# Kernel tuning notes

Hardware: AMD Instinct MI355X
Metric: run time of the kernel (lower is better)

The kernel has to match this reference:

```python
import jax, jax.numpy as jnp
import numpy as np

B, C, H, W = 8, 80, 128, 128
K = 100
MAX_OBJS = 128
N_GT = 256  # 32 GT boxes per image
HM_W, WH_W, OFF_W = 1.0, 0.1, 1.0
BETA = 0.1  # iou_map weight ('Ct IoU Loss x 0.1')


def setup_inputs() -> dict:
    key = jax.random.key(0)
    ks = jax.random.split(key, 12)
    hm = jax.random.normal(ks[0], (B, C, H, W), jnp.float32)
    wh = jax.random.normal(ks[1], (B, 2, H, W), jnp.float32) * 2.0 + 8.0
    reg = jax.random.normal(ks[2], (B, 2, H, W), jnp.float32) * 0.1
    hm_target = jax.random.uniform(ks[3], (B, C, H, W), jnp.float32) * 0.99
    wh_target = jax.random.uniform(ks[4], (B, MAX_OBJS, 2), jnp.float32) * 20.0 + 2.0
    reg_target = jax.random.uniform(ks[5], (B, MAX_OBJS, 2), jnp.float32)
    reg_mask = jax.random.randint(ks[6], (B, MAX_OBJS), 0, 2).astype(jnp.int32)
    ind = jax.random.randint(ks[7], (B, MAX_OBJS), 0, H * W).astype(jnp.int32)
    cx = jax.random.uniform(ks[8], (N_GT,)) * (W - 1)
    cy = jax.random.uniform(ks[9], (N_GT,)) * (H - 1)
    bw = jax.random.uniform(ks[10], (N_GT,)) * 30.0 + 2.0
    bh = jax.random.uniform(ks[11], (N_GT,)) * 30.0 + 2.0
    target_box = jnp.stack([cx - bw / 2, cy - bh / 2, cx + bw / 2, cy + bh / 2], -1).astype(jnp.float32)
    target_bidx = jnp.repeat(jnp.arange(B), N_GT // B).astype(jnp.int32)
    return {"hm": hm, "wh": wh, "reg": reg, "hm_target": hm_target,
            "wh_target": wh_target, "reg_target": reg_target,
            "reg_mask": reg_mask, "ind": ind,
            "target_box": target_box, "target_bidx": target_bidx}


def _gather_feat(feat, ind):
    # feat [B, ch, H, W], ind [B, M] spatial indices -> [B, M, ch]
    b, ch = feat.shape[0], feat.shape[1]
    f = feat.reshape(b, ch, -1).transpose(0, 2, 1)  # [B, HW, ch]
    return jnp.take_along_axis(f, ind[:, :, None], axis=1)


def _pairwise_iou(boxes1, boxes2):
    # boxes1 [K,4], boxes2 [N,4], xyxy -> [K,N]
    a1 = jnp.maximum(boxes1[:, 2] - boxes1[:, 0], 0.0) * jnp.maximum(boxes1[:, 3] - boxes1[:, 1], 0.0)
    a2 = jnp.maximum(boxes2[:, 2] - boxes2[:, 0], 0.0) * jnp.maximum(boxes2[:, 3] - boxes2[:, 1], 0.0)
    lt = jnp.maximum(boxes1[:, None, :2], boxes2[None, :, :2])
    rb = jnp.minimum(boxes1[:, None, 2:], boxes2[None, :, 2:])
    whi = jnp.clip(rb - lt, 0.0)
    inter = whi[..., 0] * whi[..., 1]
    union = a1[:, None] + a2[None, :] - inter
    return inter / jnp.maximum(union, 1e-7)


def _decode(hm_s, wh, reg):
    # _nms: 3x3 max-pool peak keeping
    hmax = jax.lax.reduce_window(hm_s, -jnp.inf, jax.lax.max,
                                 (1, 1, 3, 3), (1, 1, 1, 1),
                                 [(0, 0), (0, 0), (1, 1), (1, 1)])
    hm_k = jnp.where(hmax == hm_s, hm_s, 0.0)
    # global top-K over C*H*W (equivalent to per-class topK then topK-of-topK)
    scores, inds = jax.lax.top_k(hm_k.reshape(B, -1), K)
    clses = inds // (H * W)
    sinds = inds % (H * W)
    ys_i = sinds // W
    xs_i = sinds % W
    r = _gather_feat(reg, sinds)  # [B,K,2] sub-pixel offsets
    xs = xs_i.astype(jnp.float32) + r[..., 0]
    ys = ys_i.astype(jnp.float32) + r[..., 1]
    w = _gather_feat(wh, sinds)   # [B,K,2]
    boxes = jnp.stack([xs - w[..., 0] / 2, ys - w[..., 1] / 2,
                       xs + w[..., 0] / 2, ys + w[..., 1] / 2], -1)
    return boxes, scores, clses, ys_i, xs_i


def _focal_loss(pred, gt):
    # CenterNet focal loss; pred already sigmoid+clamped
    pos = gt == 1.0
    neg_w = (1.0 - gt) ** 4
    pos_loss = jnp.sum(jnp.where(pos, jnp.log(pred) * (1.0 - pred) ** 2, 0.0))
    neg_loss = jnp.sum(jnp.where(pos, 0.0, jnp.log(1.0 - pred) * pred ** 2 * neg_w))
    num_pos = jnp.sum(pos.astype(jnp.float32))
    return jnp.where(num_pos > 0, -(pos_loss + neg_loss) / jnp.maximum(num_pos, 1.0), -neg_loss)


def _reg_l1(out, mask, ind, tgt):
    pred = _gather_feat(out, ind)                       # [B, M, 2]
    m = jnp.broadcast_to(mask.astype(jnp.float32)[:, :, None], pred.shape)
    return jnp.sum(jnp.abs(pred * m - tgt * m)) / (jnp.sum(m) + 1e-4)


def reference(hm, wh, reg, hm_target, wh_target, reg_target, reg_mask, ind, target_box, target_bidx):
    hm_s = jnp.clip(jax.nn.sigmoid(hm), 1e-4, 1.0 - 1e-4)  # _sigmoid
    boxes, scores, clses, ys_i, xs_i = _decode(hm_s, wh, reg)
    # per-image pairwise IoU vs GT boxes of the same image, max over GT
    iou_all = jax.vmap(lambda bx: _pairwise_iou(bx, target_box))(boxes)  # [B,K,N]
    bmask = target_bidx[None, None, :] == jnp.arange(B)[:, None, None]
    iou = jnp.max(jnp.where(bmask, iou_all, 0.0), axis=-1)              # [B,K]
    # scatter IoU into dense heatmap-shaped iou_map at (b, cls, y, x)
    b_idx = jnp.broadcast_to(jnp.arange(B)[:, None], (B, K))
    iou_map = jnp.zeros_like(hm_s).at[b_idx, clses, ys_i, xs_i].set(iou)
    hm_t = jnp.clip(hm_target + BETA * iou_map, 0.0, 1.0)
    hm_loss = _focal_loss(hm_s, hm_t)
    wh_loss = _reg_l1(wh, reg_mask, ind, wh_target)
    off_loss = _reg_l1(reg, reg_mask, ind, reg_target)
    loss = HM_W * hm_loss + WH_W * wh_loss + OFF_W * off_loss
    return loss, hm_loss, wh_loss, off_loss
```

## Files before the change

kernel.cpp:

```cpp
#include <hip/hip_runtime.h>
#include <math.h>

#define B_ 8
#define C_ 80
#define H_ 128
#define W_ 128
#define K_ 100
#define MAXOBJS_ 128
#define NGT_ 256
#define HW_ (H_*W_)
#define CHW_ (C_*H_*W_)
#define TOT_ (B_*CHW_)
#define NBINS_ 4096
#define BCAP_ 4096
#define DCAP_ 128
#define CAPLDS_ 1024
#define DLOC_ 128
#define BLOC_ 768
#define NEGINF_ (-INFINITY)

#define OFF_MISC    64
#define OFF_LISTCNT 96
#define OFF_BDONE   128
#define OFF_SELDONE 160
#define OFF_THRB    192
#define OFF_CNTA    224
#define OFF_CNTB    256
#define OFF_HIST    512
#define ZERO_BYTES  131584
#define OFF_DEFV    131584
#define OFF_DEFI    135680
#define OFF_BORV    139776
#define OFF_BORI    270848
#define OFF_LIST    401920
#define CAP_REQ     196608ull
#define CAP_MAX     262144ull

__device__ __forceinline__ unsigned skey(float x){
    unsigned u = __float_as_uint(x);
    return (u & 0x80000000u) ? ~u : (u | 0x80000000u);
}

__device__ __forceinline__ void find_thr(const unsigned* __restrict__ lh,
                                         unsigned* __restrict__ part,
                                         unsigned target,
                                         unsigned* out_thr, unsigned* out_cum){
    int t = threadIdx.x;
    unsigned s = 0;
    #pragma unroll
    for(int k=0;k<16;++k) s += lh[t*16+k];
    part[t] = s;
    __syncthreads();
    for(int off=1; off<256; off<<=1){
        unsigned v = (t+off<256) ? part[t+off] : 0u;
        __syncthreads();
        part[t] += v;
        __syncthreads();
    }
    unsigned nxt = (t<255) ? part[t+1] : 0u;
    if(part[t] >= target && nxt < target){
        unsigned cum = nxt;
        int thr = t*16;
        for(int bin=t*16+15; bin>=t*16; --bin){
            unsigned c = lh[bin];
            if(cum + c >= target){ thr = bin; break; }
            cum += c;
        }
        *out_thr = (unsigned)thr;
        *out_cum = cum;
    }
    __syncthreads();
}

__device__ __forceinline__ void hmax4v(const float4& f, float le, float re, float h[4]){
    h[0]=fmaxf(fmaxf(le,  f.x), f.y);
    h[1]=fmaxf(fmaxf(f.x, f.y), f.z);
    h[2]=fmaxf(fmaxf(f.y, f.z), f.w);
    h[3]=fmaxf(fmaxf(f.z, f.w), re);
}

__global__ __launch_bounds__(256) void k_main(const float* __restrict__ hm,
        const float* __restrict__ hmt, unsigned* __restrict__ hist,
        double* __restrict__ accum, unsigned* __restrict__ listcnt,
        int2* __restrict__ list, int capB){
    __shared__ unsigned lh[NBINS_];
    __shared__ int2 lbuf[CAPLDS_];
    __shared__ float wsum[4];
    __shared__ unsigned lcnt, lbase;
    int t = threadIdx.x;
    int plane = blockIdx.x >> 1;
    int half  = blockIdx.x & 1;
    int b = plane / C_;
    int cls = plane - b*C_;
    const float* P = hm  + (size_t)plane*HW_;
    const float* T = hmt + (size_t)plane*HW_;
    int idx0 = cls*HW_;

    for(int i=t;i<NBINS_;i+=256) lh[i]=0u;
    if(t==0) lcnt=0u;
    __syncthreads();

    int xq = t & 31;
    int y0 = half*64 + (t>>5)*8;

    float4 rows[10];
    #pragma unroll
    for(int r=0;r<10;++r){
        int y = y0 - 1 + r;
        if(y >= 0 && y < H_) rows[r] = *(const float4*)(P + y*W_ + xq*4);
        else { rows[r].x=NEGINF_; rows[r].y=NEGINF_; rows[r].z=NEGINF_; rows[r].w=NEGINF_; }
    }
    float4 tgt[8];
    #pragma unroll
    for(int r=0;r<8;++r) tgt[r] = *(const float4*)(T + (y0+r)*W_ + xq*4);

    float le[10], re[10];
    #pragma unroll
    for(int r=0;r<10;++r){
        float l  = __shfl_up(rows[r].w, 1, 32);
        float rr = __shfl_down(rows[r].x, 1, 32);
        le[r] = (xq==0)  ? NEGINF_ : l;
        re[r] = (xq==31) ? NEGINF_ : rr;
    }

    float acc = 0.f;
    #pragma unroll
    for(int ri=0; ri<8; ++ri){
        int r = ri + 1;
        int y = y0 + ri;
        float vv[4] = {rows[r].x, rows[r].y, rows[r].z, rows[r].w};
        float hp[4]; hmax4v(rows[r-1], le[r-1], re[r-1], hp);
        float hn[4]; hmax4v(rows[r+1], le[r+1], re[r+1], hn);
        float lrv[4];
        lrv[0]=fmaxf(le[r], vv[1]);
        lrv[1]=fmaxf(vv[0], vv[2]);
        lrv[2]=fmaxf(vv[1], vv[3]);
        lrv[3]=fmaxf(vv[2], re[r]);
        float tgv[4] = {tgt[ri].x, tgt[ri].y, tgt[ri].z, tgt[ri].w};
        #pragma unroll
        for(int j=0;j<4;++j){
            float v = vv[j];
            bool pk = (v>=lrv[j]) && (v>=hp[j]) && (v>=hn[j]);
            if(pk){
                atomicAdd(&lh[skey(v)>>20], 1u);
                if(capB){
                    unsigned p = atomicAdd(&lcnt, 1u);
                    int2 e; e.x = __float_as_int(v); e.y = idx0 + y*W_ + xq*4 + j;
                    if(p < CAPLDS_) lbuf[p] = e;
                    else {
                        unsigned g = atomicAdd(&listcnt[b], 1u);
                        if(g < (unsigned)capB) list[(size_t)b*capB + g] = e;
                    }
                }
            }
            float pr = 1.f/(1.f + __expf(-v));
            pr = fminf(fmaxf(pr, 1e-4f), 1.f - 1e-4f);
            float q = 1.f - tgv[j]; float q2 = q*q;
            acc += __logf(1.f - pr) * pr * pr * q2 * q2;
        }
    }
    __syncthreads();

    unsigned n = lcnt; if(n > CAPLDS_) n = CAPLDS_;
    if(capB && t==0) lbase = atomicAdd(&listcnt[b], n);
    for(int i=t;i<NBINS_;i+=256){ unsigned c=lh[i]; if(c) atomicAdd(&hist[b*NBINS_+i], c); }
    #pragma unroll
    for(int off=32; off>0; off>>=1) acc += __shfl_xor(acc, off, 64);
    if((t & 63) == 0) wsum[t>>6] = acc;
    __syncthreads();
    if(capB){
        for(unsigned i=t;i<n;i+=256){
            unsigned g = lbase + i;
            if(g < (unsigned)capB) list[(size_t)b*capB + g] = lbuf[i];
        }
    }
    if(t==0) atomicAdd(&accum[0], (double)(wsum[0]+wsum[1]+wsum[2]+wsum[3]));
}

__global__ void k_thresh(const unsigned* __restrict__ hist, unsigned* __restrict__ thrbin){
    __shared__ unsigned lh[NBINS_];
    __shared__ unsigned part[256];
    __shared__ unsigned thrs, cums;
    int b = blockIdx.x, t = threadIdx.x;
    for(int i=t;i<NBINS_;i+=256) lh[i]=hist[b*NBINS_+i];
    if(t==0){ thrs=0u; cums=0u; }
    __syncthreads();
    find_thr(lh, part, (unsigned)K_, &thrs, &cums);
    if(t==0) thrbin[b]=thrs;
}

__global__ __launch_bounds__(256) void k_scan(const int2* __restrict__ list,
        const unsigned* __restrict__ listcnt, int capB,
        const unsigned* __restrict__ thrbin,
        unsigned* __restrict__ cntA, unsigned* __restrict__ cntB,
        float* __restrict__ defv, int* __restrict__ defi,
        float* __restrict__ borv, int* __restrict__ bori){
    __shared__ int2 dloc[DLOC_];
    __shared__ int2 bloc[BLOC_];
    __shared__ unsigned dc, bc, dbase, bbase;
    int b = blockIdx.x >> 6;
    int chunk = blockIdx.x & 63;
    int t = threadIdx.x;
    if(t==0){ dc=0u; bc=0u; }
    __syncthreads();
    unsigned thr = thrbin[b];
    unsigned n = listcnt[b]; if(n > (unsigned)capB) n = (unsigned)capB;
    for(unsigned i = chunk*256u + t; i < n; i += 64u*256u){
        int2 e = list[(size_t)b*capB + i];
        float v = __int_as_float(e.x);
        unsigned bin = skey(v) >> 20;
        if(bin > thr){
            unsigned p = atomicAdd(&dc, 1u);
            if(p < DLOC_) dloc[p] = e;
            else { unsigned g = atomicAdd(&cntA[b],1u); if(g<DCAP_){ defv[b*DCAP_+g]=v; defi[b*DCAP_+g]=e.y; } }
        } else if(bin == thr){
            unsigned p = atomicAdd(&bc, 1u);
            if(p < BLOC_) bloc[p] = e;
            else { unsigned g = atomicAdd(&cntB[b],1u); if(g<BCAP_){ borv[b*BCAP_+g]=v; bori[b*BCAP_+g]=e.y; } }
        }
    }
    __syncthreads();
    unsigned dn = dc < DLOC_ ? dc : DLOC_;
    unsigned bn = bc < BLOC_ ? bc : BLOC_;
    if(t==0){
        dbase = dn ? atomicAdd(&cntA[b], dn) : 0u;
        bbase = bn ? atomicAdd(&cntB[b], bn) : 0u;
    }
    __syncthreads();
    for(unsigned i=t;i<dn;i+=256){
        unsigned g = dbase + i;
        if(g < DCAP_){ defv[b*DCAP_+g]=__int_as_float(dloc[i].x); defi[b*DCAP_+g]=dloc[i].y; }
    }
    for(unsigned i=t;i<bn;i+=256){
        unsigned g = bbase + i;
        if(g < BCAP_){ borv[b*BCAP_+g]=__int_as_float(bloc[i].x); bori[b*BCAP_+g]=bloc[i].y; }
    }
}

__device__ __forceinline__ bool is_peak_scalar(const float* __restrict__ hm, int idx, float v){
    int w = idx & (W_-1);
    int h = (idx >> 7) & (H_-1);
    bool peak = true;
    #pragma unroll
    for(int dy=-1; dy<=1; ++dy){
        int hh = h + dy;
        if(hh < 0 || hh >= H_) continue;
        #pragma unroll
        for(int dx=-1; dx<=1; ++dx){
            if(dy==0 && dx==0) continue;
            int ww = w + dx;
            if(ww < 0 || ww >= W_) continue;
            peak = peak && (v >= __ldg(&hm[idx + dy*W_ + dx]));
        }
    }
    return peak;
}

__global__ __launch_bounds__(256) void k_collect(const float* __restrict__ hm,
        const unsigned* __restrict__ thrbin,
        unsigned* __restrict__ cntA, unsigned* __restrict__ cntB,
        float* __restrict__ defv, int* __restrict__ defi,
        float* __restrict__ borv, int* __restrict__ bori){
    int idx = blockIdx.x*256 + threadIdx.x;
    float v = hm[idx];
    if(!is_peak_scalar(hm, idx, v)) return;
    int b = idx / CHW_;
    unsigned bin = skey(v) >> 20;
    unsigned thr = thrbin[b];
    if(bin > thr){
        unsigned p = atomicAdd(&cntA[b], 1u);
        if(p < DCAP_){ defv[b*DCAP_+p] = v; defi[b*DCAP_+p] = idx - b*CHW_; }
    } else if(bin == thr){
        unsigned p = atomicAdd(&cntB[b], 1u);
        if(p < BCAP_){ borv[b*BCAP_+p] = v; bori[b*BCAP_+p] = idx - b*CHW_; }
    }
}

__global__ __launch_bounds__(256) void k_select(const float* __restrict__ hm,
        const float* __restrict__ hmt, const float* __restrict__ wh,
        const float* __restrict__ reg, const float* __restrict__ tbox,
        const int* __restrict__ tbid,
        const float* __restrict__ wht, const float* __restrict__ regt,
        const int* __restrict__ mask, const int* __restrict__ ind,
        const unsigned* __restrict__ cntA, const unsigned* __restrict__ cntB,
        const float* __restrict__ defv, const int* __restrict__ defi,
        const float* __restrict__ borv, const int* __restrict__ bori,
        double* __restrict__ accum, int* __restrict__ misc,
        unsigned* __restrict__ seldone, float* __restrict__ out){
    int b = blockIdx.x, t = threadIdx.x;
    __shared__ float gbox[NGT_][4];
    __shared__ float garea[NGT_];
    __shared__ float sv[BCAP_];
    __shared__ int   si[BCAP_];
    __shared__ unsigned h2[NBINS_];
    __shared__ unsigned t4[BCAP_];
    __shared__ unsigned part[256];
    __shared__ int  rvI[256];
    __shared__ int  sel[K_];
    __shared__ float sbx[K_][4];
    __shared__ float sa[K_];
    __shared__ int   ioui[K_];
    __shared__ float r0s[256], r1s[256], r2s[256];
    __shared__ unsigned gcnt, selc, t3c, t4c;
    __shared__ unsigned thr2s, cum2s, thr3s, need3s;
    __shared__ int wsel, amlast;

    int nA = (int)cntA[b]; if(nA>DCAP_) nA=DCAP_; if(nA>K_) nA=K_;
    int nB = (int)cntB[b]; if(nB>BCAP_) nB=BCAP_;
    int m = K_ - nA; if(m>nB) m=nB; if(m<0) m=0;

    if(t==0){ gcnt=0u; selc=(unsigned)nA; t3c=0u; t4c=0u;
              thr2s=0u; cum2s=0u; thr3s=0u; need3s=0u; }
    for(int i=t;i<NBINS_;i+=256) h2[i]=0u;
    __syncthreads();

    for(int i=t;i<NGT_;i+=256){
        if(tbid[i]==b){
            unsigned p = atomicAdd(&gcnt, 1u);
            float gx1=tbox[i*4+0], gy1=tbox[i*4+1], gx2=tbox[i*4+2], gy2=tbox[i*4+3];
            gbox[p][0]=gx1; gbox[p][1]=gy1; gbox[p][2]=gx2; gbox[p][3]=gy2;
            garea[p]=fmaxf(gx2-gx1,0.f)*fmaxf(gy2-gy1,0.f);
        }
    }
    for(int i=t;i<nB;i+=256){ sv[i]=borv[b*BCAP_+i]; si[i]=bori[b*BCAP_+i]; }
    for(int i=t;i<nA;i+=256) sel[i]=defi[b*DCAP_+i];
    __syncthreads();

    if(m>0){
        for(int i=t;i<nB;i+=256) atomicAdd(&h2[(skey(sv[i])>>8)&0xFFFu], 1u);
        __syncthreads();
        find_thr(h2, part, (unsigned)m, &thr2s, &cum2s);
        unsigned thr2 = thr2s, need2 = (unsigned)m - cum2s;
        for(int i=t;i<nB;i+=256){
            unsigned sb=(skey(sv[i])>>8)&0xFFFu;
            if(sb>thr2){ unsigned p=atomicAdd(&selc,1u); if(p<K_) sel[p]=si[i]; }
            else if(sb==thr2){ unsigned p=atomicAdd(&t3c,1u); if(p<BCAP_) t4[p]=(unsigned)i; }
        }
        __syncthreads();
        unsigned nt3=t3c; if(nt3>BCAP_) nt3=BCAP_;
        part[t]=0u;
        __syncthreads();
        for(unsigned i=t;i<nt3;i+=256) atomicAdd(&part[skey(sv[t4[i]])&0xFFu], 1u);
        __syncthreads();
        for(int off=1; off<256; off<<=1){
            unsigned v = (t+off<256)? part[t+off] : 0u;
            __syncthreads();
            part[t] += v;
            __syncthreads();
        }
        {
            unsigned nxt = (t<255)? part[t+1] : 0u;
            if(part[t] >= need2 && nxt < need2){ thr3s=(unsigned)t; need3s=need2-nxt; }
        }
        __syncthreads();
        unsigned thr3=thr3s, need3=need3s;
        for(unsigned i=t;i<nt3;i+=256){
            unsigned ci=t4[i];
            unsigned lb=skey(sv[ci])&0xFFu;
            if(lb>thr3){ unsigned p=atomicAdd(&selc,1u); if(p<K_) sel[p]=si[ci]; }
            else if(lb==thr3){ unsigned p=atomicAdd(&t4c,1u); if(p<NBINS_) h2[p]=(unsigned)si[ci]; }
        }
        __syncthreads();
        unsigned n4=t4c; if(n4>NBINS_) n4=NBINS_;
        if(need3 >= n4){
            for(unsigned i=t;i<n4;i+=256){ unsigned p=atomicAdd(&selc,1u); if(p<K_) sel[p]=(int)h2[i]; }
            __syncthreads();
        } else {
            for(unsigned it=0; it<need3; ++it){
                int bi=0x7FFFFFFF;
                for(unsigned i=t;i<n4;i+=256){ int w=(int)h2[i]; bi = (w<bi)?w:bi; }
                rvI[t]=bi;
                __syncthreads();
                for(int st=128;st>0;st>>=1){
                    if(t<st){ int w=rvI[t+st]; if(w<rvI[t]) rvI[t]=w; }
                    __syncthreads();
                }
                if(t==0){ wsel=rvI[0]; unsigned p=selc; selc=p+1u; if(p<K_) sel[p]=wsel; }
                __syncthreads();
                int w=wsel;
                for(unsigned i=t;i<n4;i+=256) if((int)h2[i]==w) h2[i]=0x7FFFFFFFu;
                __syncthreads();
            }
        }
    }
    __syncthreads();

    int nsel=(int)selc; if(nsel>K_) nsel=K_;
    for(int k=t;k<nsel;k+=256){
        int idx = sel[k];
        int cls = idx / HW_;
        int sp  = idx - cls*HW_;
        int yi = sp>>7, xi = sp&(W_-1);
        float rr0 = reg[(b*2+0)*HW_+sp], rr1 = reg[(b*2+1)*HW_+sp];
        float w0 = wh[(b*2+0)*HW_+sp],  w1 = wh[(b*2+1)*HW_+sp];
        float xs = (float)xi + rr0, ys = (float)yi + rr1;
        float x1=xs-w0*0.5f, y1=ys-w1*0.5f, x2=xs+w0*0.5f, y2=ys+w1*0.5f;
        sbx[k][0]=x1; sbx[k][1]=y1; sbx[k][2]=x2; sbx[k][3]=y2;
        sa[k] = fmaxf(x2-x1,0.f)*fmaxf(y2-y1,0.f);
        ioui[k] = 0;
    }
    __syncthreads();
    int ng = (int)gcnt; if(ng>NGT_) ng=NGT_;
    for(int pi=t; pi<nsel*ng; pi+=256){
        int k = pi / ng, g = pi - k*ng;
        float x1=sbx[k][0], y1=sbx[k][1], x2=sbx[k][2], y2=sbx[k][3];
        float ix1=fmaxf(x1,gbox[g][0]), iy1=fmaxf(y1,gbox[g][1]);
        float ix2=fminf(x2,gbox[g][2]), iy2=fminf(y2,gbox[g][3]);
        float iw=fmaxf(ix2-ix1,0.f), ih=fmaxf(iy2-iy1,0.f);
        float inter=iw*ih;
        float uni = sa[k] + garea[g] - inter;
        float iou = inter / fmaxf(uni, 1e-7f);
        atomicMax(&ioui[k], __float_as_int(iou));
    }
    __syncthreads();
    for(int k=t;k<nsel;k+=256){
        float best = __int_as_float(ioui[k]);
        int gidx = b*CHW_ + sel[k];
        float v = hm[gidx];
        float p = 1.f/(1.f + __expf(-v));
        p = fminf(fmaxf(p, 1e-4f), 1.f - 1e-4f);
        float gt0 = hmt[gidx];
        float q0 = 1.f - gt0; float q02 = q0*q0;
        float neg0 = __logf(1.f - p) * p * p * q02 * q02;
        float gt1 = fminf(gt0 + 0.1f*best, 1.f);
        if(gt1 == 1.f){
            atomicAdd(&misc[0], 1);
            float op = 1.f - p;
            atomicAdd(&accum[1], (double)(__logf(p)*op*op));
            atomicAdd(&accum[2], (double)(-neg0));
        } else {
            float q1 = 1.f - gt1; float q12 = q1*q1;
            float neg1 = __logf(1.f - p) * p * p * q12 * q12;
            atomicAdd(&accum[2], (double)(neg1 - neg0));
        }
    }

    __threadfence();
    __syncthreads();
    if(t==0){
        unsigned d = atomicAdd(seldone, 1u);
        amlast = (d == (unsigned)(B_-1));
    }
    __syncthreads();
    if(amlast){
        __threadfence();
        float whn=0.f, offn=0.f, ms=0.f;
        for(int i=t;i<B_*MAXOBJS_;i+=256){
            int bb = i >> 7;
            float mk = (float)mask[i];
            int id = ind[i];
            float p0 = wh[(bb*2+0)*HW_+id], p1 = wh[(bb*2+1)*HW_+id];
            whn += mk*(fabsf(p0 - wht[2*i]) + fabsf(p1 - wht[2*i+1]));
            float q0 = reg[(bb*2+0)*HW_+id], q1 = reg[(bb*2+1)*HW_+id];
            offn += mk*(fabsf(q0 - regt[2*i]) + fabsf(q1 - regt[2*i+1]));
            ms += 2.f*mk;
        }
        r0s[t]=whn; r1s[t]=offn; r2s[t]=ms;
        __syncthreads();
        for(int st=128; st>0; st>>=1){
            if(t<st){ r0s[t]+=r0s[t+st]; r1s[t]+=r1s[t+st]; r2s[t]+=r2s[t+st]; }
            __syncthreads();
        }
        if(t==0){
            double nb  = __hip_atomic_load(&accum[0], __ATOMIC_RELAXED, __HIP_MEMORY_SCOPE_AGENT);
            double pos = __hip_atomic_load(&accum[1], __ATOMIC_RELAXED, __HIP_MEMORY_SCOPE_AGENT);
            double nd  = __hip_atomic_load(&accum[2], __ATOMIC_RELAXED, __HIP_MEMORY_SCOPE_AGENT);
            int np = __hip_atomic_load(&misc[0], __ATOMIC_RELAXED, __HIP_MEMORY_SCOPE_AGENT);
            double neg = nb + nd;
            float hm_loss = (np > 0) ? (float)(-(pos + neg)/(double)np) : (float)(-neg);
            float msum = r2s[0];
            float wh_loss  = r0s[0] / (msum + 1e-4f);
            float off_loss = r1s[0] / (msum + 1e-4f);
            out[0] = hm_loss + 0.1f*wh_loss + off_loss;
            out[1] = hm_loss; out[2] = wh_loss; out[3] = off_loss;
        }
    }
}

extern "C" void kernel_launch(void* const* d_in, const int* in_sizes, int n_in,
                              void* d_out, int out_size, void* d_ws, size_t ws_size,
                              hipStream_t stream){
    const float* hm   = (const float*)d_in[0];
    const float* wh   = (const float*)d_in[1];
    const float* reg  = (const float*)d_in[2];
    const float* hmt  = (const float*)d_in[3];
    const float* wht  = (const float*)d_in[4];
    const float* regt = (const float*)d_in[5];
    const int*   mask = (const int*)d_in[6];
    const int*   ind  = (const int*)d_in[7];
    const float* tbox = (const float*)d_in[8];
    const int*   tbid = (const int*)d_in[9];

    char* ws = (char*)d_ws;
    double*   accum   = (double*)ws;
    int*      misc    = (int*)(ws + OFF_MISC);
    unsigned* listcnt = (unsigned*)(ws + OFF_LISTCNT);
    unsigned* seldone = (unsigned*)(ws + OFF_SELDONE);
    unsigned* thrbin  = (unsigned*)(ws + OFF_THRB);
    unsigned* cntA    = (unsigned*)(ws + OFF_CNTA);
    unsigned* cntB    = (unsigned*)(ws + OFF_CNTB);
    unsigned* hist    = (unsigned*)(ws + OFF_HIST);
    float*    defv    = (float*)(ws + OFF_DEFV);
    int*      defi    = (int*)(ws + OFF_DEFI);
    float*    borv    = (float*)(ws + OFF_BORV);
    int*      bori    = (int*)(ws + OFF_BORI);
    int2*     list    = (int2*)(ws + OFF_LIST);

    size_t capB = 0;
    if(ws_size >= (size_t)OFF_LIST + CAP_REQ*(size_t)B_*8ull){
        capB = (ws_size - (size_t)OFF_LIST) / ((size_t)B_*8ull);
        if(capB > CAP_MAX) capB = CAP_MAX;
    }

    hipMemsetAsync(ws, 0, ZERO_BYTES, stream);
    k_main<<<B_*C_*2, 256, 0, stream>>>(hm, hmt, hist, accum, listcnt, list, (int)capB);
    k_thresh<<<B_, 256, 0, stream>>>(hist, thrbin);
    if(capB){
        k_scan<<<B_*64, 256, 0, stream>>>(list, listcnt, (int)capB, thrbin,
                                          cntA, cntB, defv, defi, borv, bori);
    } else {
        k_collect<<<TOT_/256, 256, 0, stream>>>(hm, thrbin, cntA, cntB,
                                                defv, defi, borv, bori);
    }
    k_select<<<B_, 256, 0, stream>>>(hm, hmt, wh, reg, tbox, tbid,
                                     wht, regt, mask, ind, cntA, cntB,
                                     defv, defi, borv, bori, accum, misc,
                                     seldone, (float*)d_out);
    (void)in_sizes; (void)n_in; (void)out_size;
}
```

Baseline: 81.41 us.

## Split fused focal-loss and peak-detection kernel into separate kernels

The fused main kernel is split into two. k_focal is a grid-stride elementwise kernel that computes the negative focal-loss sum over hm and hm_target. k_peaks does 3x3 peak detection on quarter-plane tiles of 4 rows per thread, using a rolling row window and scalar halo loads in place of shuffles. The aim is to lower register pressure and raise occupancy and parallelism, at the cost of reading hm twice and adding one kernel launch.

```diff
diff --git a/kernel.cpp b/kernel.cpp
--- a/kernel.cpp
+++ b/kernel.cpp
@@ -14,14 +14,14 @@
 #define NBINS_ 4096
 #define BCAP_ 4096
 #define DCAP_ 128
-#define CAPLDS_ 1024
+#define QCAP_ 512
 #define DLOC_ 128
 #define BLOC_ 768
+#define FBLK_ 2048
 #define NEGINF_ (-INFINITY)
 
 #define OFF_MISC    64
 #define OFF_LISTCNT 96
-#define OFF_BDONE   128
 #define OFF_SELDONE 160
 #define OFF_THRB    192
 #define OFF_CNTA    224
@@ -72,28 +72,68 @@
     __syncthreads();
 }
 
-__device__ __forceinline__ void hmax4v(const float4& f, float le, float re, float h[4]){
-    h[0]=fmaxf(fmaxf(le,  f.x), f.y);
-    h[1]=fmaxf(fmaxf(f.x, f.y), f.z);
-    h[2]=fmaxf(fmaxf(f.y, f.z), f.w);
-    h[3]=fmaxf(fmaxf(f.z, f.w), re);
-}
-
-__global__ __launch_bounds__(256) void k_main(const float* __restrict__ hm,
-        const float* __restrict__ hmt, unsigned* __restrict__ hist,
-        double* __restrict__ accum, unsigned* __restrict__ listcnt,
+__global__ __launch_bounds__(256) void k_focal(const float* __restrict__ hm,
+        const float* __restrict__ hmt, double* __restrict__ accum){
+    __shared__ float wsum[4];
+    int t = threadIdx.x;
+    float acc = 0.f;
+    const float4* __restrict__ v4p = (const float4*)hm;
+    const float4* __restrict__ t4p = (const float4*)hmt;
+    for(int i = blockIdx.x*256 + t; i < TOT_/4; i += FBLK_*256){
+        float4 v4 = v4p[i];
+        float4 g4 = t4p[i];
+        float vv[4] = {v4.x, v4.y, v4.z, v4.w};
+        float gg[4] = {g4.x, g4.y, g4.z, g4.w};
+        #pragma unroll
+        for(int j=0;j<4;++j){
+            float v = vv[j];
+            float p = 1.f/(1.f + __expf(-v));
+            p = fminf(fmaxf(p, 1e-4f), 1.f - 1e-4f);
+            float q = 1.f - gg[j]; float q2 = q*q;
+            acc += __logf(1.f - p) * p * p * q2 * q2;
+        }
+    }
+    #pragma unroll
+    for(int off=32; off>0; off>>=1) acc += __shfl_xor(acc, off, 64);
+    if((t & 63) == 0) wsum[t>>6] = acc;
+    __syncthreads();
+    if(t==0) atomicAdd(&accum[0], (double)(wsum[0]+wsum[1]+wsum[2]+wsum[3]));
+}
+
+struct Row { float v[4]; float le, re; };
+
+__device__ __forceinline__ Row loadrow(const float* __restrict__ P, int y, int xq){
+    Row r;
+    if(y < 0 || y >= H_){
+        r.v[0]=r.v[1]=r.v[2]=r.v[3]=r.le=r.re=NEGINF_;
+        return r;
+    }
+    const float4 f = *(const float4*)(P + y*W_ + xq*4);
+    r.v[0]=f.x; r.v[1]=f.y; r.v[2]=f.z; r.v[3]=f.w;
+    r.le = (xq==0) ? NEGINF_ : P[y*W_ + xq*4 - 1];
+    r.re = (xq==31)? NEGINF_ : P[y*W_ + xq*4 + 4];
+    return r;
+}
+
+__device__ __forceinline__ void hmax4(const Row& r, float h[4]){
+    h[0]=fmaxf(fmaxf(r.le,  r.v[0]), r.v[1]);
+    h[1]=fmaxf(fmaxf(r.v[0],r.v[1]), r.v[2]);
+    h[2]=fmaxf(fmaxf(r.v[1],r.v[2]), r.v[3]);
+    h[3]=fmaxf(fmaxf(r.v[2],r.v[3]), r.re);
+}
+
+__global__ __launch_bounds__(256) void k_peaks(const float* __restrict__ hm,
+        unsigned* __restrict__ hist, unsigned* __restrict__ listcnt,
         int2* __restrict__ list, int capB){
     __shared__ unsigned lh[NBINS_];
-    __shared__ int2 lbuf[CAPLDS_];
-    __shared__ float wsum[4];
+    __shared__ int2 lbuf[QCAP_];
     __shared__ unsigned lcnt, lbase;
     int t = threadIdx.x;
-    int plane = blockIdx.x >> 1;
-    int half  = blockIdx.x & 1;
+    int plane = blockIdx.x >> 2;
+    int quad  = blockIdx.x & 3;
     int b = plane / C_;
     int cls = plane - b*C_;
-    const float* P = hm  + (size_t)plane*HW_;
-    const float* T = hmt + (size_t)plane*HW_;
+    const float* P = hm + (size_t)plane*HW_;
     int idx0 = cls*HW_;
 
     for(int i=t;i<NBINS_;i+=256) lh[i]=0u;
@@ -101,42 +141,21 @@
     __syncthreads();
 
     int xq = t & 31;
-    int y0 = half*64 + (t>>5)*8;
-
-    float4 rows[10];
+    int y0 = quad*32 + (t>>5)*4;
+    Row rp = loadrow(P, y0-1, xq);
+    Row rc = loadrow(P, y0,   xq);
+    float hp[4]; hmax4(rp, hp);
     #pragma unroll
-    for(int r=0;r<10;++r){
-        int y = y0 - 1 + r;
-        if(y >= 0 && y < H_) rows[r] = *(const float4*)(P + y*W_ + xq*4);
-        else { rows[r].x=NEGINF_; rows[r].y=NEGINF_; rows[r].z=NEGINF_; rows[r].w=NEGINF_; }
-    }
-    float4 tgt[8];
-    #pragma unroll
-    for(int r=0;r<8;++r) tgt[r] = *(const float4*)(T + (y0+r)*W_ + xq*4);
-
-    float le[10], re[10];
-    #pragma unroll
-    for(int r=0;r<10;++r){
-        float l  = __shfl_up(rows[r].w, 1, 32);
-        float rr = __shfl_down(rows[r].x, 1, 32);
-        le[r] = (xq==0)  ? NEGINF_ : l;
-        re[r] = (xq==31) ? NEGINF_ : rr;
-    }
-
-    float acc = 0.f;
-    #pragma unroll
-    for(int ri=0; ri<8; ++ri){
-        int r = ri + 1;
-        int y = y0 + ri;
-        float vv[4] = {rows[r].x, rows[r].y, rows[r].z, rows[r].w};
-        float hp[4]; hmax4v(rows[r-1], le[r-1], re[r-1], hp);
-        float hn[4]; hmax4v(rows[r+1], le[r+1], re[r+1], hn);
+    for(int rr=0; rr<4; ++rr){
+        int y = y0 + rr;
+        Row rn = loadrow(P, y+1, xq);
+        float hn[4]; hmax4(rn, hn);
+        float vv[4] = {rc.v[0], rc.v[1], rc.v[2], rc.v[3]};
         float lrv[4];
-        lrv[0]=fmaxf(le[r], vv[1]);
-        lrv[1]=fmaxf(vv[0], vv[2]);
-        lrv[2]=fmaxf(vv[1], vv[3]);
-        lrv[3]=fmaxf(vv[2], re[r]);
-        float tgv[4] = {tgt[ri].x, tgt[ri].y, tgt[ri].z, tgt[ri].w};
+        lrv[0]=fmaxf(rc.le,  vv[1]);
+        lrv[1]=fmaxf(vv[0],  vv[2]);
+        lrv[2]=fmaxf(vv[1],  vv[3]);
+        lrv[3]=fmaxf(vv[2],  rc.re);
         #pragma unroll
         for(int j=0;j<4;++j){
             float v = vv[j];
@@ -146,27 +165,23 @@
                 if(capB){
                     unsigned p = atomicAdd(&lcnt, 1u);
                     int2 e; e.x = __float_as_int(v); e.y = idx0 + y*W_ + xq*4 + j;
-                    if(p < CAPLDS_) lbuf[p] = e;
+                    if(p < QCAP_) lbuf[p] = e;
                     else {
                         unsigned g = atomicAdd(&listcnt[b], 1u);
                         if(g < (unsigned)capB) list[(size_t)b*capB + g] = e;
                     }
                 }
             }
-            float pr = 1.f/(1.f + __expf(-v));
-            pr = fminf(fmaxf(pr, 1e-4f), 1.f - 1e-4f);
-            float q = 1.f - tgv[j]; float q2 = q*q;
-            acc += __logf(1.f - pr) * pr * pr * q2 * q2;
-        }
-    }
-    __syncthreads();
-
-    unsigned n = lcnt; if(n > CAPLDS_) n = CAPLDS_;
+        }
+        #pragma unroll
+        for(int j=0;j<4;++j) hp[j] = fmaxf(lrv[j], vv[j]);
+        rc = rn;
+    }
+    __syncthreads();
+
+    unsigned n = lcnt; if(n > QCAP_) n = QCAP_;
     if(capB && t==0) lbase = atomicAdd(&listcnt[b], n);
     for(int i=t;i<NBINS_;i+=256){ unsigned c=lh[i]; if(c) atomicAdd(&hist[b*NBINS_+i], c); }
-    #pragma unroll
-    for(int off=32; off>0; off>>=1) acc += __shfl_xor(acc, off, 64);
-    if((t & 63) == 0) wsum[t>>6] = acc;
     __syncthreads();
     if(capB){
         for(unsigned i=t;i<n;i+=256){
@@ -174,7 +189,6 @@
             if(g < (unsigned)capB) list[(size_t)b*capB + g] = lbuf[i];
         }
     }
-    if(t==0) atomicAdd(&accum[0], (double)(wsum[0]+wsum[1]+wsum[2]+wsum[3]));
 }
 
 __global__ void k_thresh(const unsigned* __restrict__ hist, unsigned* __restrict__ thrbin){
@@ -513,7 +527,8 @@
     }
 
     hipMemsetAsync(ws, 0, ZERO_BYTES, stream);
-    k_main<<<B_*C_*2, 256, 0, stream>>>(hm, hmt, hist, accum, listcnt, list, (int)capB);
+    k_focal<<<FBLK_, 256, 0, stream>>>(hm, hmt, accum);
+    k_peaks<<<B_*C_*4, 256, 0, stream>>>(hm, hist, listcnt, list, (int)capB);
     k_thresh<<<B_, 256, 0, stream>>>(hist, thrbin);
     if(capB){
         k_scan<<<B_*64, 256, 0, stream>>>(list, listcnt, (int)capB, thrbin,
```

Result: slower. 118.2 us (+45.2%).
